# Performance work log

Measured on AMD Instinct MI355X. Metric: run time of the kernel, lower is better.

The kernel has to match this reference:

```python
import jax, jax.numpy as jnp
import numpy as np

EMBED_DIM = 1024
NUM_HEADS = 16
HEAD_DIM = EMBED_DIM // NUM_HEADS
B, S = 2, 2048


def setup_inputs() -> dict:
    key = jax.random.key(0)
    ks = jax.random.split(key, 11)
    f32 = jnp.float32
    return {
        "q": jax.random.normal(ks[0], (B, S, EMBED_DIM), f32),
        "k": jax.random.normal(ks[1], (B, S, EMBED_DIM), f32),
        "v": jax.random.normal(ks[2], (B, S, EMBED_DIM), f32),
        # per-head projection weights stacked over heads: [H, E, Dh]
        "Wq": jax.random.normal(ks[3], (NUM_HEADS, EMBED_DIM, HEAD_DIM), f32),
        "Wk": jax.random.normal(ks[4], (NUM_HEADS, EMBED_DIM, HEAD_DIM), f32),
        "Wv": jax.random.normal(ks[5], (NUM_HEADS, EMBED_DIM, HEAD_DIM), f32),
        "bq": jax.random.normal(ks[6], (NUM_HEADS, HEAD_DIM), f32),
        "bk": jax.random.normal(ks[7], (NUM_HEADS, HEAD_DIM), f32),
        "bv": jax.random.normal(ks[8], (NUM_HEADS, HEAD_DIM), f32),
        "Wo": jax.random.normal(ks[9], (EMBED_DIM, EMBED_DIM), f32),
        "bo": jax.random.normal(ks[10], (EMBED_DIM,), f32),
    }


def reference(q, k, v, Wq, Wk, Wv, bq, bk, bv, Wo, bo):
    scale = jnp.asarray(np.sqrt(HEAD_DIM), q.dtype)
    # batched per-head projections: [B,S,E] x [H,E,D] -> [B,H,S,D]
    Q = jnp.einsum("bse,hed->bhsd", q, Wq) + bq[None, :, None, :]
    K = jnp.einsum("bse,hed->bhsd", k, Wk) + bk[None, :, None, :]
    V = jnp.einsum("bse,hed->bhsd", v, Wv) + bv[None, :, None, :]
    # attention scores [B,H,S,S]; original applies mask to a discarded tensor,
    # so output is unmasked softmax(QK^T/scale) @ V
    att = jnp.einsum("bhsd,bhtd->bhst", Q, K) / scale
    att = jax.nn.softmax(att, axis=-1)
    ctx = jnp.einsum("bhst,bhtd->bhsd", att, V)  # [B,H,S,D]
    # concat heads (head order preserved) then output projection
    ctx = ctx.transpose(0, 2, 1, 3).reshape(ctx.shape[0], ctx.shape[2], -1)  # [B,S,E]
    return ctx @ Wo + bo
```

## Files before the change

### kernel.cpp

```cpp
#include <hip/hip_runtime.h>
#include <hip/hip_bf16.h>

typedef unsigned short u16;
typedef unsigned int   u32;
typedef _Float16 f16;
typedef __attribute__((ext_vector_type(4))) float f32x4;
typedef __attribute__((ext_vector_type(16))) float f32x16;
typedef __attribute__((ext_vector_type(8))) short s16x8;
typedef __attribute__((ext_vector_type(8))) f16 f16x8;
typedef __attribute__((ext_vector_type(2))) __fp16 fp16x2;
typedef __attribute__((ext_vector_type(4))) u16 u16x4;
typedef __attribute__((ext_vector_type(8))) u16 u16x8;
typedef __attribute__((ext_vector_type(2))) u32 u32x2;
typedef __attribute__((ext_vector_type(4))) u32 u32x4;

#define DI __device__ __forceinline__

static constexpr int Bb = 2, Ss = 2048, Hh = 16, Dd = 64, Ee = 1024;
static constexpr int Mrows = Bb * Ss;
static constexpr size_t NE = (size_t)Mrows * Ee;
static constexpr size_t WN = (size_t)Ee * Ee;
static constexpr float QSCALE = 0.125f * 1.44269504088896f;

DI float bf2f(u16 h) { u32 u = ((u32)h) << 16; return __builtin_bit_cast(float, u); }
DI u16 f2bf(float f) {
    u32 u = __builtin_bit_cast(u32, f);
    u32 r = (u + 0x7FFFu + ((u >> 16) & 1u)) >> 16;
    return (u16)r;
}
DI u16 f2h(float f) { f16 h = (f16)f; return __builtin_bit_cast(u16, h); }
DI u32 pkrtz(float a, float b) {
    fp16x2 r = __builtin_amdgcn_cvt_pkrtz(a, b);
    return __builtin_bit_cast(u32, r);
}
DI float ex2(float x) { return __builtin_amdgcn_exp2f(x); }

#define MFMA_BF(a, b, c) __builtin_amdgcn_mfma_f32_16x16x32_bf16((a), (b), (c), 0, 0, 0)
#define MFMA_F16(a, b, c) __builtin_amdgcn_mfma_f32_16x16x32_f16( \
    __builtin_bit_cast(f16x8, (a)), __builtin_bit_cast(f16x8, (b)), (c), 0, 0, 0)
#define MFMA32_BF(a, b, c) __builtin_amdgcn_mfma_f32_32x32x16_bf16((a), (b), (c), 0, 0, 0)
#define MFMA32_F16(a, b, c) __builtin_amdgcn_mfma_f32_32x32x16_f16( \
    __builtin_bit_cast(f16x8, (a)), __builtin_bit_cast(f16x8, (b)), (c), 0, 0, 0)

DI void gld16(const u16* g, u16* l) {
    __builtin_amdgcn_global_load_lds((const __attribute__((address_space(1))) void*)g,
                                     (__attribute__((address_space(3))) void*)l, 16, 0, 0);
}

__global__ __launch_bounds__(256) void k_prep(
    const float* __restrict__ q, const float* __restrict__ k, const float* __restrict__ v,
    u16* __restrict__ qh, u16* __restrict__ ql,
    u16* __restrict__ kh, u16* __restrict__ kl, u16* __restrict__ vh,
    const float* __restrict__ Wq, const float* __restrict__ Wk,
    const float* __restrict__ Wv, const float* __restrict__ Wo,
    u16* __restrict__ WqTh, u16* __restrict__ WqTl,
    u16* __restrict__ WkTh, u16* __restrict__ WkTl,
    u16* __restrict__ WvT, u16* __restrict__ WoT) {
    __shared__ float Ts[64 * 65];
    const int bid = blockIdx.x;
    if (bid < 6144) {
        const int y = bid >> 11;
        size_t i = ((size_t)(bid & 2047) * 256 + threadIdx.x) * 8;
        if (y == 2) {
            f32x4 a = *(const f32x4*)(v + i);
            f32x4 b2 = *(const f32x4*)(v + i + 4);
            u16x8 o_;
#pragma unroll
            for (int j = 0; j < 4; j++) { o_[j] = f2h(a[j]); o_[4 + j] = f2h(b2[j]); }
            *(u16x8*)(vh + i) = o_;
            return;
        }
        const float* s = y ? k : q;
        u16* h = y ? kh : qh;
        u16* l = y ? kl : ql;
        f32x4 a = *(const f32x4*)(s + i);
        f32x4 b2 = *(const f32x4*)(s + i + 4);
        u16x8 oh, ol;
#pragma unroll
        for (int j = 0; j < 4; j++) {
            u16 hh = f2bf(a[j]); oh[j] = hh; ol[j] = f2bf(a[j] - bf2f(hh));
            u16 h2 = f2bf(b2[j]); oh[4 + j] = h2; ol[4 + j] = f2bf(b2[j] - bf2f(h2));
        }
        *(u16x8*)(h + i) = oh;
        *(u16x8*)(l + i) = ol;
        return;
    }
    const int t2 = bid - 6144;
    const int y = t2 >> 8;
    const int bx = t2 & 255;
    const int ti = bx >> 4, tj = bx & 15;
    const float* W = (y == 0) ? Wq : (y == 1) ? Wk : (y == 2) ? Wv : Wo;
    const int t = threadIdx.x;
    const int col = t & 63, rb = (t >> 6) * 16;
#pragma unroll
    for (int rr = 0; rr < 16; rr++) {
        int row = rb + rr;
        float vv = (y < 3) ? W[(size_t)ti * 65536 + (size_t)(tj * 64 + row) * 64 + col]
                           : W[(size_t)(tj * 64 + row) * Ee + ti * 64 + col];
        Ts[row * 65 + col] = vv;
    }
    __syncthreads();
#pragma unroll
    for (int rr = 0; rr < 16; rr++) {
        int orow = rb + rr;
        int ocol = col;
        float vv = Ts[ocol * 65 + orow];
        size_t oidx = (size_t)(ti * 64 + orow) * Ee + tj * 64 + ocol;
        if (y == 0) {
            u16 hh = f2bf(vv); WqTh[oidx] = hh; WqTl[oidx] = f2bf(vv - bf2f(hh));
        } else if (y == 1) {
            u16 hh = f2bf(vv); WkTh[oidx] = hh; WkTl[oidx] = f2bf(vv - bf2f(hh));
        } else if (y == 2) {
            WvT[oidx] = f2h(vv);
        } else {
            WoT[oidx] = f2h(vv);
        }
    }
}

template <int SPLIT, int F16, int OUTMODE>
DI void gemm_body(const u16* __restrict__ Ah, const u16* __restrict__ Al,
                  const u16* __restrict__ Bh, const u16* __restrict__ Bl,
                  const float* __restrict__ bias,
                  u16* __restrict__ C16h, u16* __restrict__ C16l, float* __restrict__ Cf,
                  float scale, u16* As0, u16* As1, u16* Bs0, u16* Bs1) {
    constexpr int M = Mrows, N = Ee, K = Ee;
    const int tid = threadIdx.x;
    const int wave = tid >> 6, lane = tid & 63;
    const int quad = lane >> 4, l16 = lane & 15;
    const int m0 = blockIdx.y * 128, n0 = blockIdx.x * 128;
    const int wm = (wave >> 1) * 64, wn = (wave & 1) * 64;

    f32x4 acc[4][4];
#pragma unroll
    for (int i = 0; i < 4; i++)
#pragma unroll
        for (int j = 0; j < 4; j++) acc[i][j] = (f32x4)0.0f;

    for (int kk = 0; kk < K; kk += 32) {
        __syncthreads();
#pragma unroll
        for (int i = 0; i < 2; i++) {
            int c = tid + i * 256;
            int row = c >> 2, j = c & 3;
            size_t ga = (size_t)(m0 + row) * K + kk + j * 8;
            gld16(Ah + ga, As0 + c * 8);
            if constexpr (SPLIT) gld16(Al + ga, As1 + c * 8);
            size_t gb = (size_t)(n0 + row) * K + kk + j * 8;
            gld16(Bh + gb, Bs0 + c * 8);
            if constexpr (SPLIT) gld16(Bl + gb, Bs1 + c * 8);
        }
        __syncthreads();

        s16x8 bf[4][2];
#pragma unroll
        for (int nt = 0; nt < 4; nt++) {
            int r = wn + nt * 16 + l16;
            bf[nt][0] = *(const s16x8*)&Bs0[r * 32 + quad * 8];
            if constexpr (SPLIT) bf[nt][1] = *(const s16x8*)&Bs1[r * 32 + quad * 8];
        }
#pragma unroll
        for (int mt = 0; mt < 4; mt++) {
            int r = wm + mt * 16 + l16;
            s16x8 a0 = *(const s16x8*)&As0[r * 32 + quad * 8];
            s16x8 a1;
            if constexpr (SPLIT) a1 = *(const s16x8*)&As1[r * 32 + quad * 8];
#pragma unroll
            for (int nt = 0; nt < 4; nt++) {
                if constexpr (F16) {
                    acc[mt][nt] = MFMA_F16(a0, bf[nt][0], acc[mt][nt]);
                } else {
                    acc[mt][nt] = MFMA_BF(a0, bf[nt][0], acc[mt][nt]);
                    if constexpr (SPLIT) {
                        acc[mt][nt] = MFMA_BF(a0, bf[nt][1], acc[mt][nt]);
                        acc[mt][nt] = MFMA_BF(a1, bf[nt][0], acc[mt][nt]);
                    }
                }
            }
        }
    }

#pragma unroll
    for (int mt = 0; mt < 4; mt++)
#pragma unroll
        for (int nt = 0; nt < 4; nt++) {
            int gn = n0 + wn + nt * 16 + l16;
            float bs = bias[gn];
            if constexpr (OUTMODE == 1) {
                int gm = m0 + wm + mt * 16 + quad * 4;
                u16x4 pk;
#pragma unroll
                for (int r = 0; r < 4; r++) pk[r] = f2h((acc[mt][nt][r] + bs) * scale);
                *(u16x4*)&C16h[(size_t)gn * M + gm] = pk;
            } else {
#pragma unroll
                for (int r = 0; r < 4; r++) {
                    int gm = m0 + wm + mt * 16 + quad * 4 + r;
                    float v = (acc[mt][nt][r] + bs) * scale;
                    if constexpr (OUTMODE == 0) {
                        Cf[(size_t)gm * N + gn] = v;
                    } else {
                        u16 hh = f2bf(v);
                        C16h[(size_t)gm * N + gn] = hh;
                        C16l[(size_t)gm * N + gn] = f2bf(v - bf2f(hh));
                    }
                }
            }
        }
}

__global__ __launch_bounds__(256, 3) void k_qkv(
    const u16* __restrict__ qh, const u16* __restrict__ ql,
    const u16* __restrict__ kh, const u16* __restrict__ kl,
    const u16* __restrict__ vh,
    const u16* __restrict__ WqTh, const u16* __restrict__ WqTl,
    const u16* __restrict__ WkTh, const u16* __restrict__ WkTl,
    const u16* __restrict__ WvT,
    const float* __restrict__ bq, const float* __restrict__ bk, const float* __restrict__ bv,
    u16* __restrict__ Qh, u16* __restrict__ Ql2,
    u16* __restrict__ Kh, u16* __restrict__ Kl2, u16* __restrict__ Vt) {
    __shared__ u16 As[2][128 * 32];
    __shared__ u16 Bs[2][128 * 32];
    int z = blockIdx.z;
    if (z == 0)
        gemm_body<1, 0, 2>(qh, ql, WqTh, WqTl, bq, Qh, Ql2, nullptr, QSCALE,
                           As[0], As[1], Bs[0], Bs[1]);
    else if (z == 1)
        gemm_body<1, 0, 2>(kh, kl, WkTh, WkTl, bk, Kh, Kl2, nullptr, 1.0f,
                           As[0], As[1], Bs[0], Bs[1]);
    else
        gemm_body<0, 1, 1>(vh, nullptr, WvT, nullptr, bv, Vt, nullptr, nullptr, 1.0f,
                           As[0], As[1], Bs[0], Bs[1]);
}

__global__ __launch_bounds__(256, 3) void k_out(
    const u16* __restrict__ ctx, const u16* __restrict__ WoT,
    const float* __restrict__ bo, float* __restrict__ out) {
    __shared__ u16 As[128 * 32];
    __shared__ u16 Bs[128 * 32];
    gemm_body<0, 1, 0>(ctx, nullptr, WoT, nullptr, bo, nullptr, nullptr, out, 1.0f,
                       As, nullptr, Bs, nullptr);
}

__global__ __launch_bounds__(256, 2) void k_attn(
    const u16* __restrict__ Qh, const u16* __restrict__ Ql,
    const u16* __restrict__ Kh, const u16* __restrict__ Kl,
    const u16* __restrict__ Vt, u16* __restrict__ ctx) {
    const int bh = blockIdx.x;
    const int b = bh >> 4, h = bh & 15;
    const int q0 = blockIdx.y * 128;
    const int rowBase = b * Ss + q0;
    const int hc = h * 64;

    __shared__ u16 Ks[2][2][64 * 64];
    __shared__ u16 Vs[2][64 * 64];

    const int tid = threadIdx.x;
    const int wave = tid >> 6, lane = tid & 63;
    const int l31 = lane & 31, hi = lane >> 5;
    const int swl = l31 & 7;

    const int c0 = tid, c1 = tid + 256;
    const int srow0 = c0 >> 3, sj0 = (c0 & 7) ^ (srow0 & 7);
    const int srow1 = c1 >> 3, sj1 = (c1 & 7) ^ (srow1 & 7);

    auto stage = [&](int t0, int bf) {
        const size_t kb = (size_t)(b * Ss + t0) * Ee + hc;
        const size_t vb0 = (size_t)(hc + srow0) * Mrows + b * Ss + t0;
        const size_t vb1 = (size_t)(hc + srow1) * Mrows + b * Ss + t0;
        gld16(Kh + kb + (size_t)srow0 * Ee + sj0 * 8, &Ks[bf][0][c0 * 8]);
        gld16(Kh + kb + (size_t)srow1 * Ee + sj1 * 8, &Ks[bf][0][c1 * 8]);
        gld16(Kl + kb + (size_t)srow0 * Ee + sj0 * 8, &Ks[bf][1][c0 * 8]);
        gld16(Kl + kb + (size_t)srow1 * Ee + sj1 * 8, &Ks[bf][1][c1 * 8]);
        gld16(Vt + vb0 + sj0 * 8, &Vs[bf][c0 * 8]);
        gld16(Vt + vb1 + sj1 * 8, &Vs[bf][c1 * 8]);
    };

    s16x8 bqh[4], bql[4];
    {
        const size_t qoff = (size_t)(rowBase + wave * 32 + l31) * Ee + hc + hi * 8;
#pragma unroll
        for (int ks = 0; ks < 4; ks++) {
            bqh[ks] = *(const s16x8*)(Qh + qoff + ks * 16);
            bql[ks] = *(const s16x8*)(Ql + qoff + ks * 16);
        }
    }

    f32x16 o[2];
    o[0] = (f32x16)0.0f;
    o[1] = (f32x16)0.0f;
    float m_ = -1e30f, l_ = 0.f;

    stage(0, 0);
    __syncthreads();

    for (int t0 = 0; t0 < Ss; t0 += 64) {
        const int p = (t0 >> 6) & 1;
        if (t0 + 64 < Ss) stage(t0 + 64, p ^ 1);

        const u16* Kp = &Ks[p][0][0];
        const u16* Vp = &Vs[p][0];

        f32x16 st[2];
        st[0] = (f32x16)0.0f;
        st[1] = (f32x16)0.0f;
        __builtin_amdgcn_s_setprio(1);
#pragma unroll
        for (int mt = 0; mt < 2; mt++) {
            const int rb = (mt * 32 + l31) * 64;
#pragma unroll
            for (int ks = 0; ks < 4; ks++) {
                const int sj = ((2 * ks + hi) ^ swl) * 8;
                s16x8 akh = *(const s16x8*)(Kp + rb + sj);
                s16x8 akl = *(const s16x8*)(Kp + rb + sj + 4096);
                st[mt] = MFMA32_BF(akh, bqh[ks], st[mt]);
                st[mt] = MFMA32_BF(akh, bql[ks], st[mt]);
                st[mt] = MFMA32_BF(akl, bqh[ks], st[mt]);
            }
        }
        __builtin_amdgcn_s_setprio(0);

        float tmax = st[0][0];
#pragma unroll
        for (int mt = 0; mt < 2; mt++)
#pragma unroll
            for (int r = 0; r < 16; r++) tmax = fmaxf(tmax, st[mt][r]);
        tmax = fmaxf(tmax, __shfl_xor(tmax, 32));
        float mnew = fmaxf(m_, tmax);
        float al = ex2(m_ - mnew);
        m_ = mnew;
        float psum = 0.f;
#pragma unroll
        for (int mt = 0; mt < 2; mt++)
#pragma unroll
            for (int r = 0; r < 16; r++) {
                st[mt][r] = ex2(st[mt][r] - mnew);
                psum += st[mt][r];
            }
        psum += __shfl_xor(psum, 32);
        l_ = l_ * al + psum;
        o[0] *= al;
        o[1] *= al;

        s16x8 pa[4];
#pragma unroll
        for (int kt = 0; kt < 4; kt++) {
            const int G0 = 2 * kt, G1 = 2 * kt + 1;
            const int m0_ = G0 >> 2, r0_ = (G0 & 3) * 4;
            const int m1_ = G1 >> 2, r1_ = (G1 & 3) * 4;
            u32 wA0 = pkrtz(st[m0_][r0_ + 0], st[m0_][r0_ + 1]);
            u32 wB0 = pkrtz(st[m0_][r0_ + 2], st[m0_][r0_ + 3]);
            u32 wA1 = pkrtz(st[m1_][r1_ + 0], st[m1_][r1_ + 1]);
            u32 wB1 = pkrtz(st[m1_][r1_ + 2], st[m1_][r1_ + 3]);
            u32x2 rA = __builtin_amdgcn_permlane32_swap(wA0, wA1, false, false);
            u32x2 rB = __builtin_amdgcn_permlane32_swap(wB0, wB1, false, false);
            u32x4 w;
            w[0] = rA[0]; w[1] = rB[0]; w[2] = rA[1]; w[3] = rB[1];
            pa[kt] = __builtin_bit_cast(s16x8, w);
        }

        __builtin_amdgcn_s_setprio(1);
#pragma unroll
        for (int dt = 0; dt < 2; dt++) {
            const int rbv = (dt * 32 + l31) * 64;
#pragma unroll
            for (int kt = 0; kt < 4; kt++) {
                const int sj = ((2 * kt + hi) ^ swl) * 8;
                s16x8 av = *(const s16x8*)(Vp + rbv + sj);
                o[dt] = MFMA32_F16(av, pa[kt], o[dt]);
            }
        }
        __builtin_amdgcn_s_setprio(0);

        __syncthreads();
    }

    float inv = 1.0f / l_;
    const size_t obase = (size_t)(rowBase + wave * 32 + l31) * Ee + hc + hi * 4;
#pragma unroll
    for (int dt = 0; dt < 2; dt++)
#pragma unroll
        for (int g = 0; g < 4; g++) {
            u32x2 pk;
            pk[0] = pkrtz(o[dt][g * 4 + 0] * inv, o[dt][g * 4 + 1] * inv);
            pk[1] = pkrtz(o[dt][g * 4 + 2] * inv, o[dt][g * 4 + 3] * inv);
            *(u32x2*)&ctx[obase + dt * 32 + g * 8] = pk;
        }
}

extern "C" void kernel_launch(void* const* d_in, const int* in_sizes, int n_in,
                              void* d_out, int out_size, void* d_ws, size_t ws_size,
                              hipStream_t stream) {
    const float* q   = (const float*)d_in[0];
    const float* kin = (const float*)d_in[1];
    const float* v   = (const float*)d_in[2];
    const float* Wq  = (const float*)d_in[3];
    const float* Wk  = (const float*)d_in[4];
    const float* Wv  = (const float*)d_in[5];
    const float* bq  = (const float*)d_in[6];
    const float* bk  = (const float*)d_in[7];
    const float* bv  = (const float*)d_in[8];
    const float* Wo  = (const float*)d_in[9];
    const float* bo  = (const float*)d_in[10];

    u16* ws = (u16*)d_ws;
    u16 *qh = ws,          *ql = ws + NE,     *kh = ws + 2 * NE, *kl = ws + 3 * NE;
    u16 *vh = ws + 4 * NE;
    u16 *Qh = ws + 5 * NE, *Ql = ws + 6 * NE, *Kh = ws + 7 * NE, *Kl = ws + 8 * NE;
    u16 *Vt = ws + 9 * NE, *ctx = ws + 10 * NE;
    u16 *WqTh = ws + 11 * NE;
    u16 *WqTl = WqTh + WN, *WkTh = WqTh + 2 * WN, *WkTl = WqTh + 3 * WN;
    u16 *WvT = WqTh + 4 * WN, *WoT = WqTh + 5 * WN;

    dim3 b256(256);
    k_prep<<<dim3(6144 + 1024), b256, 0, stream>>>(q, kin, v, qh, ql, kh, kl, vh,
                                                   Wq, Wk, Wv, Wo,
                                                   WqTh, WqTl, WkTh, WkTl, WvT, WoT);

    k_qkv<<<dim3(8, 32, 3), b256, 0, stream>>>(qh, ql, kh, kl, vh,
                                               WqTh, WqTl, WkTh, WkTl, WvT,
                                               bq, bk, bv, Qh, Ql, Kh, Kl, Vt);

    k_attn<<<dim3(Bb * Hh, Ss / 128), b256, 0, stream>>>(Qh, Ql, Kh, Kl, Vt, ctx);

    k_out<<<dim3(8, 32), b256, 0, stream>>>(ctx, WoT, bo, (float*)d_out);
}
```

Baseline: 280.8 us.

## Split attention KV range across two blocks and merge partials with atomic counter

Splits each query tile's key/value loop into two halves handled by separate blocks (grid z=2), doubling the number of attention blocks from 512 to 1024 to fill more CUs. Each block writes unnormalized partial output plus max/sum to workspace, and the second finisher (found via an atomic counter) merges both using log-sum-exp rescaling and writes ctx. Launch bounds rise to 3 blocks per SM. This adds a memset, extra global traffic for the partials, and fences. The partials reuse the start of the workspace (the qh/ql region), which is dead after k_qkv.

```diff
diff --git a/kernel.cpp b/kernel.cpp
--- a/kernel.cpp
+++ b/kernel.cpp
@@ -242,18 +242,22 @@
                        As, nullptr, Bs, nullptr);
 }
 
-__global__ __launch_bounds__(256, 2) void k_attn(
+__global__ __launch_bounds__(256, 3) void k_attn(
     const u16* __restrict__ Qh, const u16* __restrict__ Ql,
     const u16* __restrict__ Kh, const u16* __restrict__ Kl,
-    const u16* __restrict__ Vt, u16* __restrict__ ctx) {
+    const u16* __restrict__ Vt, u16* __restrict__ ctx,
+    float* __restrict__ pO, float* __restrict__ pML, u32* __restrict__ cnt) {
     const int bh = blockIdx.x;
     const int b = bh >> 4, h = bh & 15;
     const int q0 = blockIdx.y * 128;
+    const int z = blockIdx.z;
     const int rowBase = b * Ss + q0;
     const int hc = h * 64;
+    const int tStart = z * (Ss / 2), tEnd = tStart + Ss / 2;
 
     __shared__ u16 Ks[2][2][64 * 64];
     __shared__ u16 Vs[2][64 * 64];
+    __shared__ u32 sOld;
 
     const int tid = threadIdx.x;
     const int wave = tid >> 6, lane = tid & 63;
@@ -291,12 +295,12 @@
     o[1] = (f32x16)0.0f;
     float m_ = -1e30f, l_ = 0.f;
 
-    stage(0, 0);
+    stage(tStart, 0);
     __syncthreads();
 
-    for (int t0 = 0; t0 < Ss; t0 += 64) {
+    for (int t0 = tStart; t0 < tEnd; t0 += 64) {
         const int p = (t0 >> 6) & 1;
-        if (t0 + 64 < Ss) stage(t0 + 64, p ^ 1);
+        if (t0 + 64 < tEnd) stage(t0 + 64, p ^ 1);
 
         const u16* Kp = &Ks[p][0][0];
         const u16* Vp = &Vs[p][0];
@@ -375,15 +379,39 @@
         __syncthreads();
     }
 
-    float inv = 1.0f / l_;
+    const int qt = blockIdx.y;
+    const size_t slot = ((((size_t)bh * 16 + qt) * 2 + z) * 256 + tid);
+    float* po = pO + slot * 32;
+    *(f32x16*)(po) = o[0];
+    *(f32x16*)(po + 16) = o[1];
+    pML[slot * 2 + 0] = m_;
+    pML[slot * 2 + 1] = l_;
+    __threadfence();
+    if (tid == 0) sOld = atomicAdd(&cnt[bh * 16 + qt], 1u);
+    __syncthreads();
+    if (sOld == 0) return;
+    __threadfence();
+    const size_t oslot = ((((size_t)bh * 16 + qt) * 2 + (z ^ 1)) * 256 + tid);
+    const float* qo = pO + oslot * 32;
+    f32x16 o2a = *(const f32x16*)(qo);
+    f32x16 o2b = *(const f32x16*)(qo + 16);
+    float m2 = pML[oslot * 2 + 0];
+    float l2 = pML[oslot * 2 + 1];
+    float M = fmaxf(m_, m2);
+    float w1 = ex2(m_ - M), w2 = ex2(m2 - M);
+    float inv = 1.0f / (l_ * w1 + l2 * w2);
+    w1 *= inv; w2 *= inv;
+    o[0] = o[0] * w1 + o2a * w2;
+    o[1] = o[1] * w1 + o2b * w2;
+
     const size_t obase = (size_t)(rowBase + wave * 32 + l31) * Ee + hc + hi * 4;
 #pragma unroll
     for (int dt = 0; dt < 2; dt++)
 #pragma unroll
         for (int g = 0; g < 4; g++) {
             u32x2 pk;
-            pk[0] = pkrtz(o[dt][g * 4 + 0] * inv, o[dt][g * 4 + 1] * inv);
-            pk[1] = pkrtz(o[dt][g * 4 + 2] * inv, o[dt][g * 4 + 3] * inv);
+            pk[0] = pkrtz(o[dt][g * 4 + 0], o[dt][g * 4 + 1]);
+            pk[1] = pkrtz(o[dt][g * 4 + 2], o[dt][g * 4 + 3]);
             *(u32x2*)&ctx[obase + dt * 32 + g * 8] = pk;
         }
 }
@@ -412,6 +440,10 @@
     u16 *WqTl = WqTh + WN, *WkTh = WqTh + 2 * WN, *WkTl = WqTh + 3 * WN;
     u16 *WvT = WqTh + 4 * WN, *WoT = WqTh + 5 * WN;
 
+    float* pO  = (float*)ws;
+    float* pML = (float*)(ws + ((size_t)18 << 20));
+    u32*  cnt  = (u32*) (ws + ((size_t)19 << 20));
+
     dim3 b256(256);
     k_prep<<<dim3(6144 + 1024), b256, 0, stream>>>(q, kin, v, qh, ql, kh, kl, vh,
                                                    Wq, Wk, Wv, Wo,
@@ -421,7 +453,10 @@
                                                WqTh, WqTl, WkTh, WkTl, WvT,
                                                bq, bk, bv, Qh, Ql, Kh, Kl, Vt);
 
-    k_attn<<<dim3(Bb * Hh, Ss / 128), b256, 0, stream>>>(Qh, Ql, Kh, Kl, Vt, ctx);
+    hipMemsetAsync(cnt, 0, 512 * sizeof(u32), stream);
+
+    k_attn<<<dim3(Bb * Hh, Ss / 128, 2), b256, 0, stream>>>(Qh, Ql, Kh, Kl, Vt, ctx,
+                                                            pO, pML, cnt);
 
     k_out<<<dim3(8, 32), b256, 0, stream>>>(ctx, WoT, bo, (float*)d_out);
 }
```

Result: slower. 498.1 us (+77.4%).

## Software-pipeline attention QK of next tile with softmax/PV of current tile

Applied to the files above, without the earlier changes.

Moves the attention loop to a triple-buffered K/V shared memory ring and a two-stage software pipeline. The QK^T MFMAs for tile i+1 are issued before the softmax and PV of tile i, so matrix work can overlap with the exp/max VALU work. In exchange it uses 1.5x the LDS (which may hurt occupancy at 2 blocks/CU) and keeps extra accumulator registers live.

```diff
diff --git a/kernel.cpp b/kernel.cpp
--- a/kernel.cpp
+++ b/kernel.cpp
@@ -252,8 +252,8 @@
     const int rowBase = b * Ss + q0;
     const int hc = h * 64;
 
-    __shared__ u16 Ks[2][2][64 * 64];
-    __shared__ u16 Vs[2][64 * 64];
+    __shared__ u16 Ks[3][2][64 * 64];
+    __shared__ u16 Vs[3][64 * 64];
 
     const int tid = threadIdx.x;
     const int wave = tid >> 6, lane = tid & 63;
@@ -264,16 +264,16 @@
     const int srow0 = c0 >> 3, sj0 = (c0 & 7) ^ (srow0 & 7);
     const int srow1 = c1 >> 3, sj1 = (c1 & 7) ^ (srow1 & 7);
 
-    auto stage = [&](int t0, int bf) {
+    auto stage = [&](int t0, u16* Kd, u16* Vd) {
         const size_t kb = (size_t)(b * Ss + t0) * Ee + hc;
         const size_t vb0 = (size_t)(hc + srow0) * Mrows + b * Ss + t0;
         const size_t vb1 = (size_t)(hc + srow1) * Mrows + b * Ss + t0;
-        gld16(Kh + kb + (size_t)srow0 * Ee + sj0 * 8, &Ks[bf][0][c0 * 8]);
-        gld16(Kh + kb + (size_t)srow1 * Ee + sj1 * 8, &Ks[bf][0][c1 * 8]);
-        gld16(Kl + kb + (size_t)srow0 * Ee + sj0 * 8, &Ks[bf][1][c0 * 8]);
-        gld16(Kl + kb + (size_t)srow1 * Ee + sj1 * 8, &Ks[bf][1][c1 * 8]);
-        gld16(Vt + vb0 + sj0 * 8, &Vs[bf][c0 * 8]);
-        gld16(Vt + vb1 + sj1 * 8, &Vs[bf][c1 * 8]);
+        gld16(Kh + kb + (size_t)srow0 * Ee + sj0 * 8, Kd + c0 * 8);
+        gld16(Kh + kb + (size_t)srow1 * Ee + sj1 * 8, Kd + c1 * 8);
+        gld16(Kl + kb + (size_t)srow0 * Ee + sj0 * 8, Kd + 4096 + c0 * 8);
+        gld16(Kl + kb + (size_t)srow1 * Ee + sj1 * 8, Kd + 4096 + c1 * 8);
+        gld16(Vt + vb0 + sj0 * 8, Vd + c0 * 8);
+        gld16(Vt + vb1 + sj1 * 8, Vd + c1 * 8);
     };
 
     s16x8 bqh[4], bql[4];
@@ -291,17 +291,7 @@
     o[1] = (f32x16)0.0f;
     float m_ = -1e30f, l_ = 0.f;
 
-    stage(0, 0);
-    __syncthreads();
-
-    for (int t0 = 0; t0 < Ss; t0 += 64) {
-        const int p = (t0 >> 6) & 1;
-        if (t0 + 64 < Ss) stage(t0 + 64, p ^ 1);
-
-        const u16* Kp = &Ks[p][0][0];
-        const u16* Vp = &Vs[p][0];
-
-        f32x16 st[2];
+    auto qk = [&](const u16* Kp, f32x16* st) {
         st[0] = (f32x16)0.0f;
         st[1] = (f32x16)0.0f;
         __builtin_amdgcn_s_setprio(1);
@@ -319,7 +309,9 @@
             }
         }
         __builtin_amdgcn_s_setprio(0);
-
+    };
+
+    auto finish = [&](f32x16* st, const u16* Vp) {
         float tmax = st[0][0];
 #pragma unroll
         for (int mt = 0; mt < 2; mt++)
@@ -371,9 +363,36 @@
             }
         }
         __builtin_amdgcn_s_setprio(0);
-
+    };
+
+    u16 *KA = &Ks[0][0][0], *KB = &Ks[1][0][0], *KC = &Ks[2][0][0];
+    u16 *VA = &Vs[0][0],    *VB = &Vs[1][0],    *VC = &Vs[2][0];
+
+    stage(0, KA, VA);
+    stage(64, KB, VB);
+    __syncthreads();
+
+    f32x16 stA[2], stB[2];
+    qk(KA, stA);
+
+    for (int i = 0; i < 15; ++i) {
+        const int t0 = i * 128;
+        stage(t0 + 128, KC, VC);
+        qk(KB, stB);
+        finish(stA, VA);
         __syncthreads();
-    }
+        { u16* t = KA; KA = KB; KB = KC; KC = t; }
+        { u16* t = VA; VA = VB; VB = VC; VC = t; }
+        stage(t0 + 192, KC, VC);
+        qk(KB, stA);
+        finish(stB, VA);
+        __syncthreads();
+        { u16* t = KA; KA = KB; KB = KC; KC = t; }
+        { u16* t = VA; VA = VB; VB = VC; VC = t; }
+    }
+    qk(KB, stB);
+    finish(stA, VA);
+    finish(stB, VB);
 
     float inv = 1.0f / l_;
     const size_t obase = (size_t)(rowBase + wave * 32 + l31) * Ee + hc + hi * 4;
```

Measured after the change: 274.2 us. 2.3% less time.
